# Optimization experiments

Hardware: AMD Instinct MI355X
Metric: run time of the kernel (lower is better)

## Reference

```python
import jax, jax.numpy as jnp
import numpy as np

N, E = 20000, 320000
EPS = 1e-5
NEG_SLOPE = 0.2


def gat_conv(x, src, dst, W, att_src, att_dst, bias, num_nodes):
    # W: [Fin, H*C], att_*: [H, C], bias: [H*C]
    H, C = att_src.shape
    h = (x @ W).reshape(num_nodes, H, C)            # [N,H,C]
    a_s = jnp.einsum('nhc,hc->nh', h, att_src)      # [N,H]
    a_d = jnp.einsum('nhc,hc->nh', h, att_dst)      # [N,H]
    e = jax.nn.leaky_relu(a_s[src] + a_d[dst], NEG_SLOPE)  # [E,H]
    m = jax.ops.segment_max(e, dst, num_segments=num_nodes)       # per-dst max (self-loops guarantee non-empty)
    ex = jnp.exp(e - m[dst])
    s = jax.ops.segment_sum(ex, dst, num_segments=num_nodes)
    alpha = ex / s[dst]                              # [E,H] segment softmax
    out = jax.ops.segment_sum(h[src] * alpha[:, :, None], dst, num_segments=num_nodes)  # [N,H,C]
    return out.reshape(num_nodes, H * C) + bias


def batch_norm(x, gamma, beta):
    mu = x.mean(axis=0)
    var = x.var(axis=0)  # biased, as torch BN uses for normalization
    return (x - mu) * jax.lax.rsqrt(var + EPS) * gamma + beta


def setup_inputs() -> dict:
    key = jax.random.key(0)
    ks = jax.random.split(key, 32)
    x = jax.random.normal(ks[0], (N, 512), dtype=jnp.float32)
    edge_index = jax.random.randint(ks[1], (2, E), 0, N, dtype=jnp.int32)
    d = {"x": x, "edge_index": edge_index}
    # layer configs: (Fin, C_out, H)
    cfgs = [(512, 64, 8), (512, 64, 4), (256, 64, 2), (128, 16, 1)]
    i = 2
    for li, (fin, c, h) in enumerate(cfgs, start=1):
        sc = 1.0 / np.sqrt(fin)
        d[f"W{li}"] = jax.random.normal(ks[i], (fin, h * c), dtype=jnp.float32) * sc; i += 1
        d[f"as{li}"] = jax.random.normal(ks[i], (h, c), dtype=jnp.float32) * 0.1; i += 1
        d[f"ad{li}"] = jax.random.normal(ks[i], (h, c), dtype=jnp.float32) * 0.1; i += 1
        d[f"b{li}"] = jnp.zeros((h * c,), dtype=jnp.float32)
        if li < 4:
            d[f"g{li}"] = jnp.ones((h * c,), dtype=jnp.float32)
            d[f"be{li}"] = jnp.zeros((h * c,), dtype=jnp.float32)
    return d


def reference(x, edge_index, W1, as1, ad1, b1, g1, be1, W2, as2, ad2, b2, g2, be2, W3, as3, ad3, b3, g3, be3, W4, as4, ad4, b4):
    num_nodes = x.shape[0]
    loop = jnp.arange(num_nodes, dtype=edge_index.dtype)
    src = jnp.concatenate([edge_index[0], loop])  # add_self_loops=True
    dst = jnp.concatenate([edge_index[1], loop])
    h = gat_conv(x, src, dst, W1, as1, ad1, b1, num_nodes)
    h = jax.nn.elu(batch_norm(h, g1, be1))
    h = gat_conv(h, src, dst, W2, as2, ad2, b2, num_nodes)
    h = jax.nn.elu(batch_norm(h, g2, be2))
    h = gat_conv(h, src, dst, W3, as3, ad3, b3, num_nodes)
    h = jax.nn.elu(batch_norm(h, g3, be3))
    h = gat_conv(h, src, dst, W4, as4, ad4, b4, num_nodes)
    return jax.nn.log_softmax(h, axis=1)
```

## Files before the change

kernel.cpp:

```cpp
#include <hip/hip_runtime.h>
#include <hip/hip_bf16.h>
#include <cstdint>
#include <cstddef>

#define NN 20000
#define EE 320000
#define ET (EE + NN)
#define MPAD 20096
#define BNP 256
#define SCHUNK 20

typedef __attribute__((ext_vector_type(8))) short  short8;
typedef __attribute__((ext_vector_type(4))) float  floatx4;

__device__ inline unsigned short f2bf(float f) {
    unsigned u = __float_as_uint(f);
    u += 0x7FFFu + ((u >> 16) & 1u);
    return (unsigned short)(u >> 16);
}
__device__ inline float bf2f(unsigned short b) {
    return __uint_as_float(((unsigned)b) << 16);
}
__device__ inline float bflo(unsigned u) { return __uint_as_float(u << 16); }
__device__ inline float bfhi(unsigned u) { return __uint_as_float(u & 0xFFFF0000u); }

template <int H> struct VecT;
template <> struct VecT<8> { using T = uint4; };
template <> struct VecT<4> { using T = uint2; };
template <> struct VecT<2> { using T = unsigned; };

__global__ void zero_i32(int* __restrict__ p, int n) {
    int i = blockIdx.x * blockDim.x + threadIdx.x;
    if (i < n) p[i] = 0;
}

__global__ void cvt_a_bf16(const float* __restrict__ in, unsigned short* __restrict__ out,
                           int M, int Mpad, int K) {
    long long base = ((long long)blockIdx.x * blockDim.x + threadIdx.x) * 4;
    if (base >= (long long)Mpad * K) return;
    int row = (int)(base / K);
    float4 v = make_float4(0.f, 0.f, 0.f, 0.f);
    if (row < M) v = *(const float4*)(in + base);
    ushort4 o;
    o.x = f2bf(v.x); o.y = f2bf(v.y); o.z = f2bf(v.z); o.w = f2bf(v.w);
    *(ushort4*)(out + base) = o;
}

__global__ void cvt_w_t(const float* __restrict__ W, unsigned short* __restrict__ Wt,
                        int K, int N) {
    int i = blockIdx.x * blockDim.x + threadIdx.x;
    if (i >= K * N) return;
    int k = i / N, n = i - k * N;
    Wt[(size_t)n * K + k] = f2bf(W[i]);
}

__global__ void count_edges(const int* __restrict__ dst, int* __restrict__ cnt) {
    int e = blockIdx.x * blockDim.x + threadIdx.x;
    if (e >= ET) return;
    int d = (e < EE) ? dst[e] : (e - EE);
    atomicAdd(&cnt[d], 1);
}

__global__ __launch_bounds__(1024) void scan_fast(const int* __restrict__ cnt,
                                                  int* __restrict__ rowp,
                                                  int* __restrict__ wptr, int n) {
    __shared__ int sums[1024];
    const int t = threadIdx.x;
    const int base = t * SCHUNK;
    int local[SCHUNK];
    int acc = 0;
#pragma unroll
    for (int i = 0; i < SCHUNK; ++i) {
        int idx = base + i;
        int v = (idx < n) ? cnt[idx] : 0;
        local[i] = acc;
        acc += v;
    }
    sums[t] = acc;
    __syncthreads();
    for (int o = 1; o < 1024; o <<= 1) {
        int u = (t >= o) ? sums[t - o] : 0;
        __syncthreads();
        sums[t] += u;
        __syncthreads();
    }
    int excl = sums[t] - acc;
#pragma unroll
    for (int i = 0; i < SCHUNK; ++i) {
        int idx = base + i;
        if (idx < n) { int rp = excl + local[i]; rowp[idx] = rp; wptr[idx] = rp; }
    }
    if (t == 1023) rowp[n] = sums[1023];
}

__global__ void fill_edges(const int* __restrict__ src, const int* __restrict__ dst,
                           int* __restrict__ wptr, int* __restrict__ colx) {
    int e = blockIdx.x * blockDim.x + threadIdx.x;
    if (e >= ET) return;
    int s, d;
    if (e < EE) { s = src[e]; d = dst[e]; } else { s = e - EE; d = e - EE; }
    int pos = atomicAdd(&wptr[d], 1);
    colx[pos] = s;
}

__global__ __launch_bounds__(256) void gemm_bf16_fused(
        const unsigned short* __restrict__ A, const unsigned short* __restrict__ Bt,
        unsigned short* __restrict__ hN, float* __restrict__ aS, float* __restrict__ aD,
        const float* __restrict__ atts, const float* __restrict__ attd,
        int M, int N, int K) {
    __shared__ unsigned short As[128][40];
    __shared__ unsigned short Bs[128][40];
    const int t = threadIdx.x;
    const int lane = t & 63, wave = t >> 6;
    const int wm = wave >> 1, wn = wave & 1;
    const int quad = lane >> 4, mrow = lane & 15;
    const int row0 = blockIdx.y * 128, col0 = blockIdx.x * 128;
    const int srow = t >> 2, schunk = (t & 3) * 8;
    const int H = N >> 6;

    floatx4 acc[4][4];
#pragma unroll
    for (int i = 0; i < 4; ++i)
#pragma unroll
        for (int j = 0; j < 4; ++j)
#pragma unroll
            for (int r = 0; r < 4; ++r) acc[i][j][r] = 0.f;

    for (int k0 = 0; k0 < K; k0 += 32) {
        uint4 ra0 = *(const uint4*)(A  + (size_t)(row0 + srow)      * K + k0 + schunk);
        uint4 ra1 = *(const uint4*)(A  + (size_t)(row0 + srow + 64) * K + k0 + schunk);
        uint4 rb0 = *(const uint4*)(Bt + (size_t)(col0 + srow)      * K + k0 + schunk);
        uint4 rb1 = *(const uint4*)(Bt + (size_t)(col0 + srow + 64) * K + k0 + schunk);
        __syncthreads();
        *(uint4*)&As[srow][schunk]      = ra0;
        *(uint4*)&As[srow + 64][schunk] = ra1;
        *(uint4*)&Bs[srow][schunk]      = rb0;
        *(uint4*)&Bs[srow + 64][schunk] = rb1;
        __syncthreads();

        short8 af[4], bfr[4];
#pragma unroll
        for (int i = 0; i < 4; ++i)
            af[i] = *(const short8*)&As[wm * 64 + i * 16 + mrow][quad * 8];
#pragma unroll
        for (int j = 0; j < 4; ++j)
            bfr[j] = *(const short8*)&Bs[wn * 64 + j * 16 + mrow][quad * 8];
#pragma unroll
        for (int i = 0; i < 4; ++i)
#pragma unroll
            for (int j = 0; j < 4; ++j)
                acc[i][j] = __builtin_amdgcn_mfma_f32_16x16x32_bf16(af[i], bfr[j], acc[i][j], 0, 0, 0);
    }

    const int head = (col0 + wn * 64) >> 6;
    float attS[4], attD[4];
#pragma unroll
    for (int j = 0; j < 4; ++j) {
        attS[j] = atts[head * 64 + j * 16 + mrow];
        attD[j] = attd[head * 64 + j * 16 + mrow];
    }

#pragma unroll
    for (int i = 0; i < 4; ++i) {
#pragma unroll
        for (int r = 0; r < 4; ++r) {
            int row = row0 + wm * 64 + i * 16 + quad * 4 + r;
            float ps = acc[i][0][r] * attS[0] + acc[i][1][r] * attS[1]
                     + acc[i][2][r] * attS[2] + acc[i][3][r] * attS[3];
            float pd = acc[i][0][r] * attD[0] + acc[i][1][r] * attD[1]
                     + acc[i][2][r] * attD[2] + acc[i][3][r] * attD[3];
#pragma unroll
            for (int o = 1; o < 16; o <<= 1) {
                ps += __shfl_xor(ps, o);
                pd += __shfl_xor(pd, o);
            }
            if (row < M) {
                if (mrow == 0) {
                    aS[(size_t)row * H + head] = ps;
                    aD[(size_t)row * H + head] = pd;
                }
#pragma unroll
                for (int j = 0; j < 4; ++j)
                    hN[(size_t)row * N + col0 + wn * 64 + j * 16 + mrow] = f2bf(acc[i][j][r]);
            }
        }
    }
}

template <int H>
__global__ __launch_bounds__(256) void gat_agg_all(
        const unsigned short* __restrict__ hN,
        const float* __restrict__ aS, const float* __restrict__ aD,
        const int* __restrict__ rowp, const int* __restrict__ colx,
        const float* __restrict__ bias, float* __restrict__ out, int Nn) {
    constexpr int F = H * 64;
    using V = typename VecT<H>::T;
    __shared__ float pbuf[4][64 * H];
    __shared__ int   snbuf[4][64];
    const int wave = threadIdx.x >> 6, lane = threadIdx.x & 63;
    const int n = blockIdx.x * 4 + wave;
    if (n >= Nn) return;
    const int hd = (lane * H) >> 6;
    const int chbase = lane * H;

    const int b0 = rowp[n], b1 = rowp[n + 1];

    float adv[H];
#pragma unroll
    for (int h = 0; h < H; ++h) adv[h] = aD[(size_t)n * H + h];

    float m[H], s[H];
#pragma unroll
    for (int h = 0; h < H; ++h) { m[h] = -1e30f; s[h] = 0.f; }
    for (int c0 = b0; c0 < b1; c0 += 64) {
        int cnt = min(64, b1 - c0);
        float e[H];
#pragma unroll
        for (int h = 0; h < H; ++h) e[h] = -1e30f;
        if (lane < cnt) {
            int sn = colx[c0 + lane];
#pragma unroll
            for (int h = 0; h < H; ++h) {
                float tt = aS[(size_t)sn * H + h] + adv[h];
                e[h] = (tt > 0.f) ? tt : 0.2f * tt;
            }
        }
#pragma unroll
        for (int h = 0; h < H; ++h) {
            float mc = e[h];
#pragma unroll
            for (int o = 32; o > 0; o >>= 1) mc = fmaxf(mc, __shfl_xor(mc, o));
            float nm = fmaxf(m[h], mc);
            s[h] *= __expf(m[h] - nm);
            float p = (lane < cnt) ? __expf(e[h] - nm) : 0.f;
#pragma unroll
            for (int o = 32; o > 0; o >>= 1) p += __shfl_xor(p, o);
            s[h] += p; m[h] = nm;
        }
    }
    float inv[H];
#pragma unroll
    for (int h = 0; h < H; ++h) inv[h] = 1.f / s[h];

    float acc[H];
#pragma unroll
    for (int h = 0; h < H; ++h) acc[h] = 0.f;

    for (int c0 = b0; c0 < b1; c0 += 64) {
        int cnt = min(64, b1 - c0);
        if (lane < cnt) {
            int sn = colx[c0 + lane];
            snbuf[wave][lane] = sn;
#pragma unroll
            for (int h = 0; h < H; ++h) {
                float tt = aS[(size_t)sn * H + h] + adv[h];
                tt = (tt > 0.f) ? tt : 0.2f * tt;
                pbuf[wave][lane * H + h] = __expf(tt - m[h]) * inv[h];
            }
        }
        __threadfence_block();

        int j = 0;
        for (; j + 4 <= cnt; j += 4) {
            int s0 = snbuf[wave][j],     s1 = snbuf[wave][j + 1];
            int s2 = snbuf[wave][j + 2], s3 = snbuf[wave][j + 3];
            float p0 = pbuf[wave][(j + 0) * H + hd];
            float p1 = pbuf[wave][(j + 1) * H + hd];
            float p2 = pbuf[wave][(j + 2) * H + hd];
            float p3 = pbuf[wave][(j + 3) * H + hd];
            V q0 = *(const V*)(hN + (size_t)s0 * F + chbase);
            V q1 = *(const V*)(hN + (size_t)s1 * F + chbase);
            V q2 = *(const V*)(hN + (size_t)s2 * F + chbase);
            V q3 = *(const V*)(hN + (size_t)s3 * F + chbase);
            const unsigned* u0 = (const unsigned*)&q0;
            const unsigned* u1 = (const unsigned*)&q1;
            const unsigned* u2 = (const unsigned*)&q2;
            const unsigned* u3 = (const unsigned*)&q3;
#pragma unroll
            for (int k = 0; k < H / 2; ++k) {
                acc[2 * k]     += p0 * bflo(u0[k]) + p1 * bflo(u1[k]) + p2 * bflo(u2[k]) + p3 * bflo(u3[k]);
                acc[2 * k + 1] += p0 * bfhi(u0[k]) + p1 * bfhi(u1[k]) + p2 * bfhi(u2[k]) + p3 * bfhi(u3[k]);
            }
        }
        for (; j < cnt; ++j) {
            int sj = snbuf[wave][j];
            float pj = pbuf[wave][j * H + hd];
            V q = *(const V*)(hN + (size_t)sj * F + chbase);
            const unsigned* u = (const unsigned*)&q;
#pragma unroll
            for (int k = 0; k < H / 2; ++k) {
                acc[2 * k]     += pj * bflo(u[k]);
                acc[2 * k + 1] += pj * bfhi(u[k]);
            }
        }
        __threadfence_block();
    }

#pragma unroll
    for (int h = 0; h < H; ++h)
        out[(size_t)n * F + chbase + h] = acc[h] + bias[chbase + h];
}

__global__ __launch_bounds__(256) void gemm_l4_fused(const unsigned short* __restrict__ A,
                                                     const float* __restrict__ B,
                                                     unsigned short* __restrict__ C,
                                                     float* __restrict__ aS, float* __restrict__ aD,
                                                     const float* __restrict__ atts,
                                                     const float* __restrict__ attd,
                                                     int M, int N, int K) {
    __shared__ float As[16][65];
    __shared__ float Bs[16][64];
    const int tid = threadIdx.x;
    const int tx = tid & 15, ty = tid >> 4;
    const int row0 = blockIdx.y * 64, col0 = blockIdx.x * 64;
    const int rA = tid >> 2, kq = (tid & 3) << 2;
    const int rB = tid >> 4, cq = (tid & 15) << 2;
    float acc[4][4] = {};

    for (int k0 = 0; k0 < K; k0 += 16) {
        ushort4 ha = *(const ushort4*)(A + (size_t)(row0 + rA) * K + k0 + kq);
        float4 fb = make_float4(0.f, 0.f, 0.f, 0.f);
        int bcol = col0 + cq;
        if (bcol < N) fb = *(const float4*)(B + (size_t)(k0 + rB) * N + bcol);
        As[kq + 0][rA] = bf2f(ha.x); As[kq + 1][rA] = bf2f(ha.y);
        As[kq + 2][rA] = bf2f(ha.z); As[kq + 3][rA] = bf2f(ha.w);
        *(float4*)&Bs[rB][cq] = fb;
        __syncthreads();
#pragma unroll
        for (int k = 0; k < 16; ++k) {
            float a0 = As[k][ty * 4 + 0];
            float a1 = As[k][ty * 4 + 1];
            float a2 = As[k][ty * 4 + 2];
            float a3 = As[k][ty * 4 + 3];
            float4 b = *(float4*)&Bs[k][tx * 4];
            acc[0][0] += a0 * b.x; acc[0][1] += a0 * b.y; acc[0][2] += a0 * b.z; acc[0][3] += a0 * b.w;
            acc[1][0] += a1 * b.x; acc[1][1] += a1 * b.y; acc[1][2] += a1 * b.z; acc[1][3] += a1 * b.w;
            acc[2][0] += a2 * b.x; acc[2][1] += a2 * b.y; acc[2][2] += a2 * b.z; acc[2][3] += a2 * b.w;
            acc[3][0] += a3 * b.x; acc[3][1] += a3 * b.y; acc[3][2] += a3 * b.z; acc[3][3] += a3 * b.w;
        }
        __syncthreads();
    }
    float as_part[4], ad_part[4];
#pragma unroll
    for (int i = 0; i < 4; ++i) { as_part[i] = 0.f; ad_part[i] = 0.f; }
    if (tx < 4) {
#pragma unroll
        for (int i = 0; i < 4; ++i) {
#pragma unroll
            for (int jj = 0; jj < 4; ++jj) {
                int c = tx * 4 + jj;
                as_part[i] += acc[i][jj] * atts[c];
                ad_part[i] += acc[i][jj] * attd[c];
            }
        }
    }
#pragma unroll
    for (int i = 0; i < 4; ++i) {
        float ps = as_part[i], pd = ad_part[i];
        ps += __shfl_xor(ps, 1); ps += __shfl_xor(ps, 2);
        pd += __shfl_xor(pd, 1); pd += __shfl_xor(pd, 2);
        int r = row0 + ty * 4 + i;
        if (r < M) {
            if (tx == 0) { aS[r] = ps; aD[r] = pd; }
#pragma unroll
            for (int jj = 0; jj < 4; ++jj) {
                int c = col0 + tx * 4 + jj;
                if (c < N) C[(size_t)r * N + c] = f2bf(acc[i][jj]);
            }
        }
    }
}

template <int C>
__global__ void gat_agg_l4_ls(const unsigned short* __restrict__ ht,
                              const float* __restrict__ as, const float* __restrict__ aD,
                              const int* __restrict__ rowp, const int* __restrict__ colx,
                              const float* __restrict__ bias, float* __restrict__ out, int Nn) {
    int n = blockIdx.x * 4 + (threadIdx.x >> 6);
    int lane = threadIdx.x & 63;
    if (n >= Nn) return;
    float adv = aD[n];
    int b0 = rowp[n], b1 = rowp[n + 1];

    float m = -1e30f, s = 0.f, acc = 0.f;
    for (int c0 = b0; c0 < b1; c0 += 64) {
        int cnt = b1 - c0; if (cnt > 64) cnt = 64;
        int sn = 0; float e = -1e30f;
        if (lane < cnt) {
            sn = colx[c0 + lane];
            float tt = as[sn] + adv;
            e = (tt > 0.f) ? tt : 0.2f * tt;
        }
        float mc = e;
#pragma unroll
        for (int o = 32; o > 0; o >>= 1) mc = fmaxf(mc, __shfl_xor(mc, o));
        float nm = fmaxf(m, mc);
        float sc = __expf(m - nm);
        acc *= sc; s *= sc;
        float p = (lane < cnt) ? __expf(e - nm) : 0.f;
        float ps = p;
#pragma unroll
        for (int o = 32; o > 0; o >>= 1) ps += __shfl_xor(ps, o);
        s += ps; m = nm;

        int j = 0;
        for (; j + 4 <= cnt; j += 4) {
            int s0 = __shfl(sn, j),     s1 = __shfl(sn, j + 1);
            int s2 = __shfl(sn, j + 2), s3 = __shfl(sn, j + 3);
            float p0 = __shfl(p, j),     p1 = __shfl(p, j + 1);
            float p2 = __shfl(p, j + 2), p3 = __shfl(p, j + 3);
            float h0 = 0.f, h1 = 0.f, h2 = 0.f, h3 = 0.f;
            if (lane < C) {
                h0 = bf2f(ht[(size_t)s0 * C + lane]);
                h1 = bf2f(ht[(size_t)s1 * C + lane]);
                h2 = bf2f(ht[(size_t)s2 * C + lane]);
                h3 = bf2f(ht[(size_t)s3 * C + lane]);
            }
            acc += p0 * h0 + p1 * h1 + p2 * h2 + p3 * h3;
        }
        for (; j < cnt; ++j) {
            int sj = __shfl(sn, j);
            float pj = __shfl(p, j);
            float hv = (lane < C) ? bf2f(ht[(size_t)sj * C + lane]) : 0.f;
            acc += pj * hv;
        }
    }
    float v = (lane < C) ? (acc / s + bias[lane]) : -1e30f;
    float mx = v;
#pragma unroll
    for (int o = 8; o > 0; o >>= 1) mx = fmaxf(mx, __shfl_xor(mx, o));
    float ex = (lane < C) ? __expf(v - mx) : 0.f;
#pragma unroll
    for (int o = 8; o > 0; o >>= 1) ex += __shfl_xor(ex, o);
    float l = __logf(ex) + mx;
    if (lane < C) out[(size_t)n * C + lane] = v - l;
}

template <int F>
__global__ __launch_bounds__(256) void bn_stats_det(const float* __restrict__ x,
                                                    float* __restrict__ part,
                                                    long long total) {
    constexpr int R  = 1024 / F;
    constexpr int NT = F / 4;
    __shared__ float sd[256 * 9];
    const int t = threadIdx.x;
    long long idx = ((long long)blockIdx.x * 256 + t) * 4;
    const long long stride = (long long)gridDim.x * 1024;
    float s0 = 0, s1 = 0, s2 = 0, s3 = 0, q0 = 0, q1 = 0, q2 = 0, q3 = 0;
    for (; idx < total; idx += stride) {
        float4 v = *(const float4*)(x + idx);
        s0 += v.x; q0 += v.x * v.x;
        s1 += v.y; q1 += v.y * v.y;
        s2 += v.z; q2 += v.z * v.z;
        s3 += v.w; q3 += v.w * v.w;
    }
    sd[t * 9 + 0] = s0; sd[t * 9 + 1] = s1; sd[t * 9 + 2] = s2; sd[t * 9 + 3] = s3;
    sd[t * 9 + 4] = q0; sd[t * 9 + 5] = q1; sd[t * 9 + 6] = q2; sd[t * 9 + 7] = q3;
    __syncthreads();
    if (t < NT) {
        float a[8];
#pragma unroll
        for (int k = 0; k < 8; ++k) a[k] = sd[t * 9 + k];
        for (int r = 1; r < R; ++r)
#pragma unroll
            for (int k = 0; k < 8; ++k) a[k] += sd[(t + r * NT) * 9 + k];
        int col = t * 4;
        float* pb = part + (size_t)blockIdx.x * 2 * F;
#pragma unroll
        for (int k = 0; k < 4; ++k) {
            pb[col + k]     = a[k];
            pb[F + col + k] = a[4 + k];
        }
    }
}

template <int F>
__global__ __launch_bounds__(256) void bn_reduce_par(const float* __restrict__ part,
                                                     const float* __restrict__ gamma,
                                                     const float* __restrict__ beta,
                                                     float* __restrict__ ss,
                                                     float invN) {
    __shared__ float sd[8][33];
    const int t = threadIdx.x;
    const int pr = t >> 5;
    const int tg = t & 31;
    const int c0 = blockIdx.x * 16;
    const int col = (tg < 16) ? (c0 + tg) : (F + c0 + (tg - 16));
    float a = 0.f;
    for (int p = pr; p < BNP; p += 8)
        a += part[(size_t)p * 2 * F + col];
    sd[pr][tg] = a;
    __syncthreads();
    if (pr == 0) {
        float tot = sd[0][tg];
#pragma unroll
        for (int r = 1; r < 8; ++r) tot += sd[r][tg];
        sd[0][tg] = tot;
    }
    __syncthreads();
    if (t < 16) {
        int c = c0 + t;
        float s = sd[0][t];
        float q = sd[0][16 + t];
        float mu = s * invN;
        float var = q * invN - mu * mu;
        float sc = gamma[c] * rsqrtf(var + 1e-5f);
        ss[c] = sc;
        ss[F + c] = beta[c] - mu * sc;
    }
}

__global__ void bn_apply_elu_bf16(const float* __restrict__ x, const float* __restrict__ ss,
                                  unsigned short* __restrict__ outA,
                                  int Nn, int F, int fmask) {
    long long idx4 = ((long long)blockIdx.x * blockDim.x + threadIdx.x) * 4;
    int row = (int)(idx4 / F);
    ushort4 o = make_ushort4(0, 0, 0, 0);
    if (row < Nn) {
        int c = (int)(idx4 & fmask);
        float4 v = *(const float4*)(x + idx4);
        float v0 = v.x * ss[c + 0] + ss[F + c + 0];
        float v1 = v.y * ss[c + 1] + ss[F + c + 1];
        float v2 = v.z * ss[c + 2] + ss[F + c + 2];
        float v3 = v.w * ss[c + 3] + ss[F + c + 3];
        v0 = (v0 > 0.f) ? v0 : (__expf(v0) - 1.f);
        v1 = (v1 > 0.f) ? v1 : (__expf(v1) - 1.f);
        v2 = (v2 > 0.f) ? v2 : (__expf(v2) - 1.f);
        v3 = (v3 > 0.f) ? v3 : (__expf(v3) - 1.f);
        o.x = f2bf(v0); o.y = f2bf(v1); o.z = f2bf(v2); o.w = f2bf(v3);
    }
    *(ushort4*)(outA + idx4) = o;
}

extern "C" void kernel_launch(void* const* d_in, const int* in_sizes, int n_in,
                              void* d_out, int out_size, void* d_ws, size_t ws_size,
                              hipStream_t stream) {
    const float* x   = (const float*)d_in[0];
    const int*   ei  = (const int*)d_in[1];
    const float* W1  = (const float*)d_in[2];
    const float* as1 = (const float*)d_in[3];
    const float* ad1 = (const float*)d_in[4];
    const float* b1  = (const float*)d_in[5];
    const float* ga1 = (const float*)d_in[6];
    const float* be1 = (const float*)d_in[7];
    const float* W2  = (const float*)d_in[8];
    const float* as2 = (const float*)d_in[9];
    const float* ad2 = (const float*)d_in[10];
    const float* b2  = (const float*)d_in[11];
    const float* ga2 = (const float*)d_in[12];
    const float* be2 = (const float*)d_in[13];
    const float* W3  = (const float*)d_in[14];
    const float* as3 = (const float*)d_in[15];
    const float* ad3 = (const float*)d_in[16];
    const float* b3  = (const float*)d_in[17];
    const float* ga3 = (const float*)d_in[18];
    const float* be3 = (const float*)d_in[19];
    const float* W4  = (const float*)d_in[20];
    const float* as4 = (const float*)d_in[21];
    const float* ad4 = (const float*)d_in[22];
    const float* b4  = (const float*)d_in[23];
    float* outp = (float*)d_out;

    uint8_t* base = (uint8_t*)d_ws;
    size_t off = 0;
    auto alloc = [&](size_t nbytes) -> void* {
        off = (off + 255) & ~(size_t)255;
        void* p = base + off;
        off += nbytes;
        return p;
    };
    float* bufO = (float*)alloc((size_t)NN * 512 * 4);
    unsigned short* bufA = (unsigned short*)alloc((size_t)MPAD * 512 * 2);
    unsigned short* hN   = (unsigned short*)alloc((size_t)NN * 512 * 2);
    unsigned short* Wt1  = (unsigned short*)alloc((size_t)512 * 512 * 2);
    unsigned short* Wt2  = (unsigned short*)alloc((size_t)256 * 512 * 2);
    unsigned short* Wt3  = (unsigned short*)alloc((size_t)128 * 256 * 2);
    float* aSn  = (float*)alloc((size_t)NN * 8 * 4);
    float* aDn  = (float*)alloc((size_t)NN * 8 * 4);
    int*   cnt  = (int*)alloc((size_t)NN * 4);
    int*   rowp = (int*)alloc((size_t)(NN + 1) * 4);
    int*   wptr = (int*)alloc((size_t)NN * 4);
    int*   colx = (int*)alloc((size_t)ET * 4);
    float* bnp  = (float*)alloc((size_t)BNP * 1024 * 4);
    float* bns  = (float*)alloc((size_t)1024 * 4);

    const int* srcRow = ei;
    const int* dstRow = ei + EE;

    zero_i32<<<(NN + 255) / 256, 256, 0, stream>>>(cnt, NN);
    count_edges<<<(ET + 255) / 256, 256, 0, stream>>>(dstRow, cnt);
    scan_fast<<<1, 1024, 0, stream>>>(cnt, rowp, wptr, NN);
    fill_edges<<<(ET + 255) / 256, 256, 0, stream>>>(srcRow, dstRow, wptr, colx);

    cvt_w_t<<<(512 * 512 + 255) / 256, 256, 0, stream>>>(W1, Wt1, 512, 512);
    cvt_w_t<<<(512 * 256 + 255) / 256, 256, 0, stream>>>(W2, Wt2, 512, 256);
    cvt_w_t<<<(256 * 128 + 255) / 256, 256, 0, stream>>>(W3, Wt3, 256, 128);

    {
        cvt_a_bf16<<<((MPAD * 512 / 4) + 255) / 256, 256, 0, stream>>>(x, bufA, NN, MPAD, 512);
        dim3 g(512 / 128, MPAD / 128);
        gemm_bf16_fused<<<g, 256, 0, stream>>>(bufA, Wt1, hN, aSn, aDn, as1, ad1, NN, 512, 512);
        gat_agg_all<8><<<NN / 4, 256, 0, stream>>>(hN, aSn, aDn, rowp, colx, b1, bufO, NN);
        bn_stats_det<512><<<BNP, 256, 0, stream>>>(bufO, bnp, (long long)NN * 512);
        bn_reduce_par<512><<<512 / 16, 256, 0, stream>>>(bnp, ga1, be1, bns, 1.0f / NN);
        bn_apply_elu_bf16<<<(MPAD * 512 / 4) / 256, 256, 0, stream>>>(bufO, bns, bufA, NN, 512, 511);
    }
    {
        dim3 g(256 / 128, MPAD / 128);
        gemm_bf16_fused<<<g, 256, 0, stream>>>(bufA, Wt2, hN, aSn, aDn, as2, ad2, NN, 256, 512);
        gat_agg_all<4><<<NN / 4, 256, 0, stream>>>(hN, aSn, aDn, rowp, colx, b2, bufO, NN);
        bn_stats_det<256><<<BNP, 256, 0, stream>>>(bufO, bnp, (long long)NN * 256);
        bn_reduce_par<256><<<256 / 16, 256, 0, stream>>>(bnp, ga2, be2, bns, 1.0f / NN);
        bn_apply_elu_bf16<<<(MPAD * 256 / 4) / 256, 256, 0, stream>>>(bufO, bns, bufA, NN, 256, 255);
    }
    {
        dim3 g(128 / 128, MPAD / 128);
        gemm_bf16_fused<<<g, 256, 0, stream>>>(bufA, Wt3, hN, aSn, aDn, as3, ad3, NN, 128, 256);
        gat_agg_all<2><<<NN / 4, 256, 0, stream>>>(hN, aSn, aDn, rowp, colx, b3, bufO, NN);
        bn_stats_det<128><<<BNP, 256, 0, stream>>>(bufO, bnp, (long long)NN * 128);
        bn_reduce_par<128><<<128 / 16, 256, 0, stream>>>(bnp, ga3, be3, bns, 1.0f / NN);
        bn_apply_elu_bf16<<<(MPAD * 128 / 4) / 256, 256, 0, stream>>>(bufO, bns, bufA, NN, 128, 127);
    }
    {
        dim3 g(1, (NN + 63) / 64);
        gemm_l4_fused<<<g, 256, 0, stream>>>(bufA, W4, hN, aSn, aDn, as4, ad4, NN, 16, 128);
        gat_agg_l4_ls<16><<<(NN + 3) / 4, 256, 0, stream>>>(hN, aSn, aDn, rowp, colx, b4, outp, NN);
    }
}
```

Baseline: 468.2 us.

## Split GAT aggregation per head with single-pass online softmax

Replaces the per-node aggregation kernel, which made two passes over each neighbour list, with one that runs a wave per (node, head). It uses a single-pass online softmax that rescales the running accumulators and broadcasts neighbour ids and weights with shuffles instead of shared memory. Attention logits are stored head-major so each head's source scores sit in one contiguous array, and the block index is swizzled so the blocks for a node group's heads are adjacent, aiming at L2 reuse. This cuts the duplicate pass over neighbour lists and raises parallelism. In exchange it re-reads rowp/colx once per head, and each lane loads only 8 bytes of features per edge. The layer-4 path is untouched, but its kernels may still read the old node-major layout.

```diff
diff --git a/kernel.cpp b/kernel.cpp
--- a/kernel.cpp
+++ b/kernel.cpp
@@ -23,11 +23,6 @@
 }
 __device__ inline float bflo(unsigned u) { return __uint_as_float(u << 16); }
 __device__ inline float bfhi(unsigned u) { return __uint_as_float(u & 0xFFFF0000u); }
-
-template <int H> struct VecT;
-template <> struct VecT<8> { using T = uint4; };
-template <> struct VecT<4> { using T = uint2; };
-template <> struct VecT<2> { using T = unsigned; };
 
 __global__ void zero_i32(int* __restrict__ p, int n) {
     int i = blockIdx.x * blockDim.x + threadIdx.x;
@@ -116,7 +111,6 @@
     const int quad = lane >> 4, mrow = lane & 15;
     const int row0 = blockIdx.y * 128, col0 = blockIdx.x * 128;
     const int srow = t >> 2, schunk = (t & 3) * 8;
-    const int H = N >> 6;
 
     floatx4 acc[4][4];
 #pragma unroll
@@ -176,8 +170,8 @@
             }
             if (row < M) {
                 if (mrow == 0) {
-                    aS[(size_t)row * H + head] = ps;
-                    aD[(size_t)row * H + head] = pd;
+                    aS[(size_t)head * M + row] = ps;
+                    aD[(size_t)head * M + row] = pd;
                 }
 #pragma unroll
                 for (int j = 0; j < 4; ++j)
@@ -187,118 +181,82 @@
     }
 }
 
-template <int H>
-__global__ __launch_bounds__(256) void gat_agg_all(
+template <int HH>
+__global__ __launch_bounds__(256) void gat_agg_head(
         const unsigned short* __restrict__ hN,
         const float* __restrict__ aS, const float* __restrict__ aD,
         const int* __restrict__ rowp, const int* __restrict__ colx,
         const float* __restrict__ bias, float* __restrict__ out, int Nn) {
-    constexpr int F = H * 64;
-    using V = typename VecT<H>::T;
-    __shared__ float pbuf[4][64 * H];
-    __shared__ int   snbuf[4][64];
+    constexpr int F = HH * 64;
+    constexpr int G = 8 / HH;
+    const int L = blockIdx.x;
+    const int x8 = L & 7;
+    const int hd = x8 / G;
+    const int nodeblk = (L >> 3) * G + (x8 & (G - 1));
     const int wave = threadIdx.x >> 6, lane = threadIdx.x & 63;
-    const int n = blockIdx.x * 4 + wave;
+    const int n = nodeblk * 4 + wave;
     if (n >= Nn) return;
-    const int hd = (lane * H) >> 6;
-    const int chbase = lane * H;
-
+
+    const float* aSh = aS + (size_t)hd * Nn;
+    const float adv = aD[(size_t)hd * Nn + n];
     const int b0 = rowp[n], b1 = rowp[n + 1];
-
-    float adv[H];
-#pragma unroll
-    for (int h = 0; h < H; ++h) adv[h] = aD[(size_t)n * H + h];
-
-    float m[H], s[H];
-#pragma unroll
-    for (int h = 0; h < H; ++h) { m[h] = -1e30f; s[h] = 0.f; }
+    const unsigned short* hbase = hN + hd * 64;
+
+    const int grp = lane >> 4;
+    const int q   = lane & 15;
+
+    float m = -1e30f, s = 0.f;
+    float a0 = 0.f, a1 = 0.f, a2 = 0.f, a3 = 0.f;
+
     for (int c0 = b0; c0 < b1; c0 += 64) {
         int cnt = min(64, b1 - c0);
-        float e[H];
-#pragma unroll
-        for (int h = 0; h < H; ++h) e[h] = -1e30f;
+        int sn = 0; float e = -1e30f;
         if (lane < cnt) {
-            int sn = colx[c0 + lane];
-#pragma unroll
-            for (int h = 0; h < H; ++h) {
-                float tt = aS[(size_t)sn * H + h] + adv[h];
-                e[h] = (tt > 0.f) ? tt : 0.2f * tt;
-            }
-        }
-#pragma unroll
-        for (int h = 0; h < H; ++h) {
-            float mc = e[h];
-#pragma unroll
-            for (int o = 32; o > 0; o >>= 1) mc = fmaxf(mc, __shfl_xor(mc, o));
-            float nm = fmaxf(m[h], mc);
-            s[h] *= __expf(m[h] - nm);
-            float p = (lane < cnt) ? __expf(e[h] - nm) : 0.f;
-#pragma unroll
-            for (int o = 32; o > 0; o >>= 1) p += __shfl_xor(p, o);
-            s[h] += p; m[h] = nm;
-        }
-    }
-    float inv[H];
-#pragma unroll
-    for (int h = 0; h < H; ++h) inv[h] = 1.f / s[h];
-
-    float acc[H];
-#pragma unroll
-    for (int h = 0; h < H; ++h) acc[h] = 0.f;
-
-    for (int c0 = b0; c0 < b1; c0 += 64) {
-        int cnt = min(64, b1 - c0);
-        if (lane < cnt) {
-            int sn = colx[c0 + lane];
-            snbuf[wave][lane] = sn;
-#pragma unroll
-            for (int h = 0; h < H; ++h) {
-                float tt = aS[(size_t)sn * H + h] + adv[h];
-                tt = (tt > 0.f) ? tt : 0.2f * tt;
-                pbuf[wave][lane * H + h] = __expf(tt - m[h]) * inv[h];
-            }
-        }
-        __threadfence_block();
-
-        int j = 0;
-        for (; j + 4 <= cnt; j += 4) {
-            int s0 = snbuf[wave][j],     s1 = snbuf[wave][j + 1];
-            int s2 = snbuf[wave][j + 2], s3 = snbuf[wave][j + 3];
-            float p0 = pbuf[wave][(j + 0) * H + hd];
-            float p1 = pbuf[wave][(j + 1) * H + hd];
-            float p2 = pbuf[wave][(j + 2) * H + hd];
-            float p3 = pbuf[wave][(j + 3) * H + hd];
-            V q0 = *(const V*)(hN + (size_t)s0 * F + chbase);
-            V q1 = *(const V*)(hN + (size_t)s1 * F + chbase);
-            V q2 = *(const V*)(hN + (size_t)s2 * F + chbase);
-            V q3 = *(const V*)(hN + (size_t)s3 * F + chbase);
-            const unsigned* u0 = (const unsigned*)&q0;
-            const unsigned* u1 = (const unsigned*)&q1;
-            const unsigned* u2 = (const unsigned*)&q2;
-            const unsigned* u3 = (const unsigned*)&q3;
-#pragma unroll
-            for (int k = 0; k < H / 2; ++k) {
-                acc[2 * k]     += p0 * bflo(u0[k]) + p1 * bflo(u1[k]) + p2 * bflo(u2[k]) + p3 * bflo(u3[k]);
-                acc[2 * k + 1] += p0 * bfhi(u0[k]) + p1 * bfhi(u1[k]) + p2 * bfhi(u2[k]) + p3 * bfhi(u3[k]);
-            }
-        }
-        for (; j < cnt; ++j) {
-            int sj = snbuf[wave][j];
-            float pj = pbuf[wave][j * H + hd];
-            V q = *(const V*)(hN + (size_t)sj * F + chbase);
-            const unsigned* u = (const unsigned*)&q;
-#pragma unroll
-            for (int k = 0; k < H / 2; ++k) {
-                acc[2 * k]     += pj * bflo(u[k]);
-                acc[2 * k + 1] += pj * bfhi(u[k]);
-            }
-        }
-        __threadfence_block();
-    }
-
-#pragma unroll
-    for (int h = 0; h < H; ++h)
-        out[(size_t)n * F + chbase + h] = acc[h] + bias[chbase + h];
+            sn = colx[c0 + lane];
+            float tt = aSh[sn] + adv;
+            e = (tt > 0.f) ? tt : 0.2f * tt;
+        }
+        float mc = e;
+#pragma unroll
+        for (int o = 32; o > 0; o >>= 1) mc = fmaxf(mc, __shfl_xor(mc, o));
+        float nm = fmaxf(m, mc);
+        float sc = __expf(m - nm);
+        float p = (lane < cnt) ? __expf(e - nm) : 0.f;
+        float ps = p;
+#pragma unroll
+        for (int o = 32; o > 0; o >>= 1) ps += __shfl_xor(ps, o);
+        s = s * sc + ps;
+        a0 *= sc; a1 *= sc; a2 *= sc; a3 *= sc;
+        m = nm;
+
+        for (int j = 0; j < cnt; j += 4) {
+            int   sg = __shfl(sn, j + grp);
+            float pg = __shfl(p,  j + grp);
+            uint2 v = *((const uint2*)(hbase + (size_t)sg * F) + q);
+            a0 += pg * bflo(v.x);
+            a1 += pg * bfhi(v.x);
+            a2 += pg * bflo(v.y);
+            a3 += pg * bfhi(v.y);
+        }
+    }
+
+#pragma unroll
+    for (int o = 16; o < 64; o <<= 1) {
+        a0 += __shfl_xor(a0, o);
+        a1 += __shfl_xor(a1, o);
+        a2 += __shfl_xor(a2, o);
+        a3 += __shfl_xor(a3, o);
+    }
+    if (lane < 16) {
+        float inv = 1.f / s;
+        int cb = hd * 64 + lane * 4;
+        float4 o4;
+        o4.x = a0 * inv + bias[cb + 0];
+        o4.y = a1 * inv + bias[cb + 1];
+        o4.z = a2 * inv + bias[cb + 2];
+        o4.w = a3 * inv + bias[cb + 3];
+        *(float4*)(out + (size_t)n * F + cb) = o4;
+    }
 }
 
 __global__ __launch_bounds__(256) void gemm_l4_fused(const unsigned short* __restrict__ A,
@@ -600,7 +558,7 @@
         cvt_a_bf16<<<((MPAD * 512 / 4) + 255) / 256, 256, 0, stream>>>(x, bufA, NN, MPAD, 512);
         dim3 g(512 / 128, MPAD / 128);
         gemm_bf16_fused<<<g, 256, 0, stream>>>(bufA, Wt1, hN, aSn, aDn, as1, ad1, NN, 512, 512);
-        gat_agg_all<8><<<NN / 4, 256, 0, stream>>>(hN, aSn, aDn, rowp, colx, b1, bufO, NN);
+        gat_agg_head<8><<<(NN / 4) * 8, 256, 0, stream>>>(hN, aSn, aDn, rowp, colx, b1, bufO, NN);
         bn_stats_det<512><<<BNP, 256, 0, stream>>>(bufO, bnp, (long long)NN * 512);
         bn_reduce_par<512><<<512 / 16, 256, 0, stream>>>(bnp, ga1, be1, bns, 1.0f / NN);
         bn_apply_elu_bf16<<<(MPAD * 512 / 4) / 256, 256, 0, stream>>>(bufO, bns, bufA, NN, 512, 511);
@@ -608,7 +566,7 @@
     {
         dim3 g(256 / 128, MPAD / 128);
         gemm_bf16_fused<<<g, 256, 0, stream>>>(bufA, Wt2, hN, aSn, aDn, as2, ad2, NN, 256, 512);
-        gat_agg_all<4><<<NN / 4, 256, 0, stream>>>(hN, aSn, aDn, rowp, colx, b2, bufO, NN);
+        gat_agg_head<4><<<(NN / 4) * 4, 256, 0, stream>>>(hN, aSn, aDn, rowp, colx, b2, bufO, NN);
         bn_stats_det<256><<<BNP, 256, 0, stream>>>(bufO, bnp, (long long)NN * 256);
         bn_reduce_par<256><<<256 / 16, 256, 0, stream>>>(bnp, ga2, be2, bns, 1.0f / NN);
         bn_apply_elu_bf16<<<(MPAD * 256 / 4) / 256, 256, 0, stream>>>(bufO, bns, bufA, NN, 256, 255);
@@ -616,7 +574,7 @@
     {
         dim3 g(128 / 128, MPAD / 128);
         gemm_bf16_fused<<<g, 256, 0, stream>>>(bufA, Wt3, hN, aSn, aDn, as3, ad3, NN, 128, 256);
-        gat_agg_all<2><<<NN / 4, 256, 0, stream>>>(hN, aSn, aDn, rowp, colx, b3, bufO, NN);
+        gat_agg_head<2><<<(NN / 4) * 2, 256, 0, stream>>>(hN, aSn, aDn, rowp, colx, b3, bufO, NN);
         bn_stats_det<128><<<BNP, 256, 0, stream>>>(bufO, bnp, (long long)NN * 128);
         bn_reduce_par<128><<<128 / 16, 256, 0, stream>>>(bnp, ga3, be3, bns, 1.0f / NN);
         bn_apply_elu_bf16<<<(MPAD * 128 / 4) / 256, 256, 0, stream>>>(bufO, bns, bufA, NN, 128, 127);
```

New measurement: 504.1 us. 7.7% more time.
